# Kernel optimization log

Measured on AMD Instinct MI355X. Metric: run time of the kernel, lower is better.

The kernel has to match this reference:

```python
import jax, jax.numpy as jnp
import numpy as np

D_MODEL = 1024
N_HEADS = 16
HEAD_DIM = D_MODEL // N_HEADS


def setup_inputs() -> dict:
    key = jax.random.key(0)
    k_x, k_qkv, k_out = jax.random.split(key, 3)
    B, T = 4, 2048
    x = jax.random.normal(k_x, (B, T, D_MODEL), dtype=jnp.float32)
    # Linear(bias=False): y = x @ W, with W stored as [in, out]
    W_qkv = jax.random.normal(k_qkv, (D_MODEL, 3 * D_MODEL), dtype=jnp.float32) * (D_MODEL ** -0.5)
    W_out = jax.random.normal(k_out, (D_MODEL, D_MODEL), dtype=jnp.float32) * (D_MODEL ** -0.5)
    return {"x": x, "W_qkv": W_qkv, "W_out": W_out}


def reference(x, W_qkv, W_out):
    B, T, C = x.shape
    H, Dh = N_HEADS, HEAD_DIM
    scale = 1.0 / jnp.sqrt(jnp.asarray(Dh, dtype=x.dtype))

    qkv = x @ W_qkv  # [B,T,3C]
    q, k, v = jnp.split(qkv, 3, axis=-1)

    def split_heads(t):
        return t.reshape(B, T, H, Dh).transpose(0, 2, 1, 3)  # [B,H,T,Dh]

    q, k, v = split_heads(q), split_heads(k), split_heads(v)

    scores = jnp.einsum('bhqd,bhkd->bhqk', q, k) * scale  # [B,H,T,T]
    causal = jnp.tril(jnp.ones((T, T), dtype=bool))
    scores = jnp.where(causal, scores, jnp.asarray(-jnp.inf, dtype=scores.dtype))
    attn = jax.nn.softmax(scores, axis=-1)
    # dropout p=0.0 -> identity
    out = jnp.einsum('bhqk,bhkd->bhqd', attn, v)  # [B,H,T,Dh]
    out = out.transpose(0, 2, 1, 3).reshape(B, T, C)
    return out @ W_out
```

## Files before the change

### kernel.cpp

```cpp
#include <hip/hip_runtime.h>
#include <stdint.h>

typedef unsigned short u16;
typedef float f32x4 __attribute__((ext_vector_type(4)));
typedef short s16x8 __attribute__((ext_vector_type(8)));

#define SEQ 2048
#define DM 1024
#define NH 16
#define HD 64
#define BATCH 4
#define ROWS (BATCH*SEQ)
#define QTILES (SEQ/64)

__device__ __forceinline__ u16 f32_bf16(float f) {
  union { float f; uint32_t u; } c; c.f = f;
  uint32_t u = c.u;
  return (u16)((u + 0x7fffu + ((u >> 16) & 1u)) >> 16);
}
__device__ __forceinline__ u16 f32_bf16_trunc(float f) {
  union { float f; uint32_t u; } c; c.f = f;
  return (u16)(c.u >> 16);
}

#define GLOAD_LDS16(g, l) __builtin_amdgcn_global_load_lds( \
    (__attribute__((address_space(1))) void*)(g),           \
    (__attribute__((address_space(3))) void*)(l), 16, 0, 0)

__global__ __launch_bounds__(256) void cast_bf16_k(const float* __restrict__ in,
                                                   u16* __restrict__ out, int n4) {
  int i = blockIdx.x * 256 + threadIdx.x;
  if (i >= n4) return;
  float4 v = ((const float4*)in)[i];
  ushort4 o;
  o.x = f32_bf16(v.x); o.y = f32_bf16(v.y); o.z = f32_bf16(v.z); o.w = f32_bf16(v.w);
  ((ushort4*)out)[i] = o;
}

__global__ __launch_bounds__(256) void cast_transpose_k(const float* __restrict__ in,
                                                        u16* __restrict__ out, int R, int C) {
  __shared__ float tile[32][33];
  int c0 = blockIdx.x * 32, r0 = blockIdx.y * 32;
  int t = threadIdx.x;
  int lr = t >> 3, lc = (t & 7) * 4;
  float4 v = *(const float4*)(in + (size_t)(r0 + lr) * C + c0 + lc);
  tile[lr][lc] = v.x; tile[lr][lc + 1] = v.y; tile[lr][lc + 2] = v.z; tile[lr][lc + 3] = v.w;
  __syncthreads();
  ushort4 o;
  o.x = f32_bf16(tile[lc + 0][lr]);
  o.y = f32_bf16(tile[lc + 1][lr]);
  o.z = f32_bf16(tile[lc + 2][lr]);
  o.w = f32_bf16(tile[lc + 3][lr]);
  *(ushort4*)(out + (size_t)(c0 + lr) * R + r0 + lc) = o;
}

#define QSCALE 0.18033688011112042f


__device__ __forceinline__ f32x4 mfma16(s16x8 a, s16x8 b, f32x4 c) {
  return __builtin_amdgcn_mfma_f32_16x16x32_bf16(a, b, c, 0, 0, 0);
}

template<int STG, int ENDVM>
__device__ __forceinline__ void tile_body(
    const u16* lAc, const u16* lBc, u16* lAs, u16* lBs,
    const u16* gA0, const u16* gA1, const u16* gB0, const u16* gB1,
    int d0, int d1, int aoff, int boff, f32x4 (&acc)[8][4])
{
  s16x8 af[4], bfr[4];
#pragma unroll
  for (int ni = 0; ni < 4; ++ni) bfr[ni] = *(const s16x8*)&lBc[boff + ni * 512];
#pragma unroll
  for (int mi = 0; mi < 4; ++mi) af[mi] = *(const s16x8*)&lAc[aoff + mi * 512];
  if (STG) { GLOAD_LDS16(gA0, lAs + d0); GLOAD_LDS16(gA1, lAs + d1); }
  __builtin_amdgcn_s_barrier();
  asm volatile("s_waitcnt lgkmcnt(0)" ::: "memory");
  __builtin_amdgcn_sched_barrier(0);
  __builtin_amdgcn_s_setprio(1);
#pragma unroll
  for (int mi = 0; mi < 4; ++mi)
#pragma unroll
    for (int ni = 0; ni < 4; ++ni)
      acc[mi][ni] = mfma16(af[mi], bfr[ni], acc[mi][ni]);
  __builtin_amdgcn_s_setprio(0);
  __builtin_amdgcn_sched_barrier(0);
  __builtin_amdgcn_s_barrier();
#pragma unroll
  for (int mi = 0; mi < 4; ++mi) af[mi] = *(const s16x8*)&lAc[aoff + 2048 + mi * 512];
  if (STG) { GLOAD_LDS16(gB0, lBs + d0); GLOAD_LDS16(gB1, lBs + d1); }
  __builtin_amdgcn_s_barrier();
  asm volatile("s_waitcnt lgkmcnt(0)" ::: "memory");
  __builtin_amdgcn_sched_barrier(0);
  __builtin_amdgcn_s_setprio(1);
#pragma unroll
  for (int mi = 0; mi < 4; ++mi)
#pragma unroll
    for (int ni = 0; ni < 4; ++ni)
      acc[4 + mi][ni] = mfma16(af[mi], bfr[ni], acc[4 + mi][ni]);
  __builtin_amdgcn_s_setprio(0);
  __builtin_amdgcn_sched_barrier(0);
  if (ENDVM == 8)      asm volatile("s_waitcnt vmcnt(8)" ::: "memory");
  else if (ENDVM == 4) asm volatile("s_waitcnt vmcnt(4)" ::: "memory");
  else if (ENDVM == 0) asm volatile("s_waitcnt vmcnt(0)" ::: "memory");
  __builtin_amdgcn_s_barrier();
  __builtin_amdgcn_sched_barrier(0);
}

__global__ __launch_bounds__(512, 2) void qkv_gemm(
    const u16* __restrict__ A, const u16* __restrict__ Bt,
    u16* __restrict__ Qo, u16* __restrict__ Ko, u16* __restrict__ Vo)
{
  __shared__ u16 lA[4][8192];
  __shared__ u16 lB[4][8192];
  int t = threadIdx.x;

  int flat = blockIdx.y * 12 + blockIdx.x;
  int swz = (flat & 7) * 48 + (flat >> 3);
  int by = swz / 12, bx = swz - by * 12;
  int m0 = by * 256, n0 = bx * 256;

  int lane = t & 63, w = t >> 6;
  int m16 = lane & 15, quad = lane >> 4;
  int wm = w >> 2, wn = w & 3;

  int r0 = t >> 2;
  int scol = ((t & 3) ^ ((t >> 3) & 3)) * 8;
  const u16* Ag0 = A  + (size_t)(m0 + r0) * DM + scol;
  const u16* Ag1 = A  + (size_t)(m0 + 128 + r0) * DM + scol;
  const u16* Bg0 = Bt + (size_t)(n0 + r0) * DM + scol;
  const u16* Bg1 = Bt + (size_t)(n0 + 128 + r0) * DM + scol;
  int d0 = t * 8, d1 = 4096 + t * 8;

  int ka = (quad ^ ((m16 >> 1) & 3)) * 8;
  int aoff = (wm * 128 + m16) * 32 + ka;
  int boff = (wn * 64 + m16) * 32 + ka;

  f32x4 acc[8][4];
#pragma unroll
  for (int mi = 0; mi < 8; ++mi)
#pragma unroll
    for (int ni = 0; ni < 4; ++ni)
#pragma unroll
      for (int r = 0; r < 4; ++r) acc[mi][ni][r] = 0.f;

#pragma unroll
  for (int kt = 0; kt < 3; ++kt) {
    GLOAD_LDS16(Ag0 + kt * 32, lA[kt] + d0);
    GLOAD_LDS16(Ag1 + kt * 32, lA[kt] + d1);
    GLOAD_LDS16(Bg0 + kt * 32, lB[kt] + d0);
    GLOAD_LDS16(Bg1 + kt * 32, lB[kt] + d1);
  }
  asm volatile("s_waitcnt vmcnt(8)" ::: "memory");
  __builtin_amdgcn_s_barrier();
  __builtin_amdgcn_sched_barrier(0);

  for (int T = 0; T <= 28; ++T) {
    int cur = T & 3, stg = (T + 3) & 3;
    tile_body<1, 8>(lA[cur], lB[cur], lA[stg], lB[stg],
                    Ag0 + (T + 3) * 32, Ag1 + (T + 3) * 32,
                    Bg0 + (T + 3) * 32, Bg1 + (T + 3) * 32,
                    d0, d1, aoff, boff, acc);
  }
  tile_body<0, 4>(lA[1], lB[1], lA[0], lB[0], Ag0, Ag1, Bg0, Bg1, d0, d1, aoff, boff, acc);
  tile_body<0, 0>(lA[2], lB[2], lA[0], lB[0], Ag0, Ag1, Bg0, Bg1, d0, d1, aoff, boff, acc);
  tile_body<0, -1>(lA[3], lB[3], lA[0], lB[0], Ag0, Ag1, Bg0, Bg1, d0, d1, aoff, boff, acc);

#pragma unroll
  for (int mi = 0; mi < 8; ++mi) {
    int gr = m0 + wm * 128 + mi * 16 + quad * 4;
    int b = gr >> 11, tt = gr & 2047;
#pragma unroll
    for (int ni = 0; ni < 4; ++ni) {
      int gc = n0 + wn * 64 + ni * 16 + m16;
      int sec = gc >> 10, rem = gc & 1023, h = rem >> 6, d = rem & 63;
      if (sec == 0) {
#pragma unroll
        for (int r = 0; r < 4; ++r)
          Qo[(((size_t)b * NH + h) * SEQ + tt + r) * HD + d] = f32_bf16(acc[mi][ni][r] * QSCALE);
      } else if (sec == 1) {
#pragma unroll
        for (int r = 0; r < 4; ++r)
          Ko[(((size_t)b * NH + h) * SEQ + tt + r) * HD + d] = f32_bf16(acc[mi][ni][r]);
      } else {
        ushort4 o;
        o.x = f32_bf16(acc[mi][ni][0]); o.y = f32_bf16(acc[mi][ni][1]);
        o.z = f32_bf16(acc[mi][ni][2]); o.w = f32_bf16(acc[mi][ni][3]);
        *(ushort4*)&Vo[(((size_t)b * NH + h) * HD + d) * SEQ + tt] = o;
      }
    }
  }
}

template<int EPI>
__global__ __launch_bounds__(256) void gemm_bt(
    const u16* __restrict__ A, const u16* __restrict__ Bt,
    float* __restrict__ Cf, u16* __restrict__ Qo, u16* __restrict__ Ko, u16* __restrict__ Vo,
    int M, int N, int K)
{
  __shared__ u16 As[128 * 32];
  __shared__ u16 Bs[128 * 32];
  int t = threadIdx.x;
  int m0 = blockIdx.y * 128, n0 = blockIdx.x * 128;

  int srow = t >> 2, scol8 = (t & 3) * 8;
  const u16* Ag0 = A  + (size_t)(m0 + srow) * K + scol8;
  const u16* Ag1 = A  + (size_t)(m0 + 64 + srow) * K + scol8;
  const u16* Bg0 = Bt + (size_t)(n0 + srow) * K + scol8;
  const u16* Bg1 = Bt + (size_t)(n0 + 64 + srow) * K + scol8;
  u16* Al0 = As + t * 8;  u16* Al1 = As + 2048 + t * 8;
  u16* Bl0 = Bs + t * 8;  u16* Bl1 = Bs + 2048 + t * 8;

  int lane = t & 63, w = t >> 6;
  int m16 = lane & 15, quad = lane >> 4;
  int wr = (w >> 1) * 64, wc = (w & 1) * 64;

  f32x4 acc[4][4];
#pragma unroll
  for (int mi = 0; mi < 4; ++mi)
#pragma unroll
    for (int ni = 0; ni < 4; ++ni)
#pragma unroll
      for (int r = 0; r < 4; ++r) acc[mi][ni][r] = 0.f;

  for (int k0 = 0; k0 < K; k0 += 32) {
    __syncthreads();
    GLOAD_LDS16(Ag0 + k0, Al0);
    GLOAD_LDS16(Ag1 + k0, Al1);
    GLOAD_LDS16(Bg0 + k0, Bl0);
    GLOAD_LDS16(Bg1 + k0, Bl1);
    __syncthreads();
    s16x8 af[4], bf[4];
#pragma unroll
    for (int mi = 0; mi < 4; ++mi)
      af[mi] = *(const s16x8*)(As + (wr + mi * 16 + m16) * 32 + quad * 8);
#pragma unroll
    for (int ni = 0; ni < 4; ++ni)
      bf[ni] = *(const s16x8*)(Bs + (wc + ni * 16 + m16) * 32 + quad * 8);
#pragma unroll
    for (int mi = 0; mi < 4; ++mi)
#pragma unroll
      for (int ni = 0; ni < 4; ++ni)
        acc[mi][ni] = __builtin_amdgcn_mfma_f32_16x16x32_bf16(af[mi], bf[ni], acc[mi][ni], 0, 0, 0);
  }

  if (EPI == 0) {
#pragma unroll
    for (int mi = 0; mi < 4; ++mi) {
      int gr = m0 + wr + mi * 16 + quad * 4;
#pragma unroll
      for (int ni = 0; ni < 4; ++ni) {
        int gc = n0 + wc + ni * 16 + m16;
#pragma unroll
        for (int r = 0; r < 4; ++r)
          Cf[(size_t)(gr + r) * N + gc] = acc[mi][ni][r];
      }
    }
  } else {
#pragma unroll
    for (int mi = 0; mi < 4; ++mi) {
      int gr = m0 + wr + mi * 16 + quad * 4;
      int b = gr >> 11, tt = gr & 2047;
#pragma unroll
      for (int ni = 0; ni < 4; ++ni) {
        int gc = n0 + wc + ni * 16 + m16;
        int sec = gc >> 10, rem = gc & 1023, h = rem >> 6, d = rem & 63;
        if (sec == 0) {
#pragma unroll
          for (int r = 0; r < 4; ++r)
            Qo[(((size_t)b * NH + h) * SEQ + tt + r) * HD + d] = f32_bf16(acc[mi][ni][r] * QSCALE);
        } else if (sec == 1) {
#pragma unroll
          for (int r = 0; r < 4; ++r)
            Ko[(((size_t)b * NH + h) * SEQ + tt + r) * HD + d] = f32_bf16(acc[mi][ni][r]);
        } else {
          ushort4 o;
          o.x = f32_bf16(acc[mi][ni][0]); o.y = f32_bf16(acc[mi][ni][1]);
          o.z = f32_bf16(acc[mi][ni][2]); o.w = f32_bf16(acc[mi][ni][3]);
          *(ushort4*)&Vo[(((size_t)b * NH + h) * HD + d) * SEQ + tt] = o;
        }
      }
    }
  }
}

__global__ __launch_bounds__(256) void attn_k(
    const u16* __restrict__ Q, const u16* __restrict__ K,
    const u16* __restrict__ Vt_g,
    u16* __restrict__ O)
{
  __shared__ u16 Ks[64][72];
  __shared__ u16 Vt[64][72];
  __shared__ u16 Ps[4][16][72];
  int bh = blockIdx.y;
  int t = threadIdx.x, w = t >> 6, lane = t & 63;
  int m16 = lane & 15, quad = lane >> 4;
  int b = bh >> 4, h = bh & 15;

  int srow = t >> 2, sc = (t & 3) * 16;
  const u16* Kg0 = K    + ((size_t)bh * SEQ + srow) * HD  + sc;
  const u16* Vg0 = Vt_g + ((size_t)bh * HD  + srow) * SEQ + sc;

  for (int half = 0; half < 2; ++half) {
    int qt = half ? (QTILES - 1 - (int)blockIdx.x) : (int)blockIdx.x;
    int q0 = qt * 64;

    const u16* Qb = Q + ((size_t)bh * SEQ + q0 + w * 16 + m16) * HD + quad * 8;
    s16x8 qf0 = *(const s16x8*)Qb;
    s16x8 qf1 = *(const s16x8*)(Qb + 32);

    f32x4 acco[4];
    float l_part[4];
#pragma unroll
    for (int r = 0; r < 4; ++r) l_part[r] = 0.f;
#pragma unroll
    for (int ni = 0; ni < 4; ++ni)
#pragma unroll
      for (int r = 0; r < 4; ++r) acco[ni][r] = 0.f;

    for (int kt = 0; kt <= qt; ++kt) {
      uint4 kv0 = *(const uint4*)(Kg0 + (size_t)kt * 64 * HD);
      uint4 kv1 = *(const uint4*)(Kg0 + (size_t)kt * 64 * HD + 8);
      uint4 vv0 = *(const uint4*)(Vg0 + kt * 64);
      uint4 vv1 = *(const uint4*)(Vg0 + kt * 64 + 8);
      __syncthreads();
      *(uint4*)&Ks[srow][sc]     = kv0;
      *(uint4*)&Ks[srow][sc + 8] = kv1;
      *(uint4*)&Vt[srow][sc]     = vv0;
      *(uint4*)&Vt[srow][sc + 8] = vv1;
      __syncthreads();

      f32x4 sacc[4];
#pragma unroll
      for (int ni = 0; ni < 4; ++ni)
#pragma unroll
        for (int r = 0; r < 4; ++r) sacc[ni][r] = 0.f;
#pragma unroll
      for (int ni = 0; ni < 4; ++ni) {
        s16x8 kf0 = *(const s16x8*)&Ks[ni * 16 + m16][quad * 8];
        s16x8 kf1 = *(const s16x8*)&Ks[ni * 16 + m16][32 + quad * 8];
        sacc[ni] = __builtin_amdgcn_mfma_f32_16x16x32_bf16(qf0, kf0, sacc[ni], 0, 0, 0);
        sacc[ni] = __builtin_amdgcn_mfma_f32_16x16x32_bf16(qf1, kf1, sacc[ni], 0, 0, 0);
      }
      if (kt == qt) {
#pragma unroll
        for (int ni = 0; ni < 4; ++ni)
#pragma unroll
          for (int r = 0; r < 4; ++r)
            if (ni * 16 + m16 > w * 16 + quad * 4 + r) sacc[ni][r] = -1e30f;
      }

#pragma unroll
      for (int ni = 0; ni < 4; ++ni)
#pragma unroll
        for (int r = 0; r < 4; ++r) {
          float p = __builtin_amdgcn_exp2f(sacc[ni][r]);
          l_part[r] += p;
          Ps[w][quad * 4 + r][ni * 16 + m16] = f32_bf16_trunc(p);
        }

#pragma unroll
      for (int ks = 0; ks < 2; ++ks) {
        s16x8 pf = *(const s16x8*)&Ps[w][m16][ks * 32 + quad * 8];
#pragma unroll
        for (int ni = 0; ni < 4; ++ni) {
          s16x8 vf = *(const s16x8*)&Vt[ni * 16 + m16][ks * 32 + quad * 8];
          acco[ni] = __builtin_amdgcn_mfma_f32_16x16x32_bf16(pf, vf, acco[ni], 0, 0, 0);
        }
      }
    }

    float l[4];
#pragma unroll
    for (int r = 0; r < 4; ++r) l[r] = l_part[r];
#pragma unroll
    for (int off = 1; off < 16; off <<= 1)
#pragma unroll
      for (int r = 0; r < 4; ++r) l[r] += __shfl_xor(l[r], off, 64);

#pragma unroll
    for (int r = 0; r < 4; ++r) {
      float inv = 1.f / l[r];
      int trow = q0 + w * 16 + quad * 4 + r;
      size_t base = ((size_t)(b * SEQ + trow)) * DM + h * HD;
#pragma unroll
      for (int ni = 0; ni < 4; ++ni)
        O[base + ni * 16 + m16] = f32_bf16(acco[ni][r] * inv);
    }
  }
}

extern "C" void kernel_launch(void* const* d_in, const int* in_sizes, int n_in,
                              void* d_out, int out_size, void* d_ws, size_t ws_size,
                              hipStream_t stream) {
  const float* x    = (const float*)d_in[0];
  const float* Wqkv = (const float*)d_in[1];
  const float* Wout = (const float*)d_in[2];
  float* out = (float*)d_out;

  u16* ws = (u16*)d_ws;
  size_t off = 0;
  u16* x_bf   = ws + off; off += (size_t)ROWS * DM;
  u16* wqkv_t = ws + off; off += (size_t)(3 * DM) * DM;
  u16* wout_t = ws + off; off += (size_t)DM * DM;
  u16* Qb     = ws + off; off += (size_t)BATCH * NH * SEQ * HD;
  u16* Kb     = ws + off; off += (size_t)BATCH * NH * SEQ * HD;
  u16* Vb     = ws + off; off += (size_t)BATCH * NH * SEQ * HD;
  u16* AO     = ws + off; off += (size_t)ROWS * DM;

  cast_bf16_k<<<(ROWS * DM / 4 + 255) / 256, 256, 0, stream>>>(x, x_bf, ROWS * DM / 4);
  cast_transpose_k<<<dim3(3 * DM / 32, DM / 32), 256, 0, stream>>>(Wqkv, wqkv_t, DM, 3 * DM);
  cast_transpose_k<<<dim3(DM / 32, DM / 32), 256, 0, stream>>>(Wout, wout_t, DM, DM);
  qkv_gemm<<<dim3(12, 32), 512, 0, stream>>>(x_bf, wqkv_t, Qb, Kb, Vb);
  attn_k<<<dim3(QTILES / 2, BATCH * NH), 256, 0, stream>>>(Qb, Kb, Vb, AO);
  gemm_bt<0><<<dim3(DM / 128, ROWS / 128), 256, 0, stream>>>(
      AO, wout_t, out, nullptr, nullptr, nullptr, ROWS, DM, DM);
}
```

Before: 288.4 us.

## Prefetch next tile's LDS fragments across K-steps in QKV GEMM

```diff
diff --git a/kernel.cpp b/kernel.cpp
--- a/kernel.cpp
+++ b/kernel.cpp
@@ -61,48 +61,56 @@
   return __builtin_amdgcn_mfma_f32_16x16x32_bf16(a, b, c, 0, 0, 0);
 }
 
-template<int STG, int ENDVM>
-__device__ __forceinline__ void tile_body(
-    const u16* lAc, const u16* lBc, u16* lAs, u16* lBs,
+template<int STG, int ENDVM, int LAST>
+__device__ __forceinline__ void tile_step(
+    const u16* lAc, const u16* lBc,
+    const u16* lAn, const u16* lBn,
+    u16* lAs, u16* lBs,
     const u16* gA0, const u16* gA1, const u16* gB0, const u16* gB1,
-    int d0, int d1, int aoff, int boff, f32x4 (&acc)[8][4])
+    int d0, int d1, int aoff, int boff,
+    s16x8 (&fa)[4], s16x8 (&fb)[4],
+    s16x8 (&na)[4], s16x8 (&nb)[4],
+    f32x4 (&acc)[8][4])
 {
-  s16x8 af[4], bfr[4];
-#pragma unroll
-  for (int ni = 0; ni < 4; ++ni) bfr[ni] = *(const s16x8*)&lBc[boff + ni * 512];
-#pragma unroll
-  for (int mi = 0; mi < 4; ++mi) af[mi] = *(const s16x8*)&lAc[aoff + mi * 512];
+  __builtin_amdgcn_s_barrier();
+  __builtin_amdgcn_sched_barrier(0);
+  s16x8 f1[4];
+#pragma unroll
+  for (int mi = 0; mi < 4; ++mi) f1[mi] = *(const s16x8*)&lAc[aoff + 2048 + mi * 512];
   if (STG) { GLOAD_LDS16(gA0, lAs + d0); GLOAD_LDS16(gA1, lAs + d1); }
-  __builtin_amdgcn_s_barrier();
-  asm volatile("s_waitcnt lgkmcnt(0)" ::: "memory");
+  asm volatile("s_waitcnt lgkmcnt(4)" ::: "memory");
   __builtin_amdgcn_sched_barrier(0);
   __builtin_amdgcn_s_setprio(1);
 #pragma unroll
   for (int mi = 0; mi < 4; ++mi)
 #pragma unroll
     for (int ni = 0; ni < 4; ++ni)
-      acc[mi][ni] = mfma16(af[mi], bfr[ni], acc[mi][ni]);
+      acc[mi][ni] = mfma16(fa[mi], fb[ni], acc[mi][ni]);
   __builtin_amdgcn_s_setprio(0);
   __builtin_amdgcn_sched_barrier(0);
-  __builtin_amdgcn_s_barrier();
-#pragma unroll
-  for (int mi = 0; mi < 4; ++mi) af[mi] = *(const s16x8*)&lAc[aoff + 2048 + mi * 512];
   if (STG) { GLOAD_LDS16(gB0, lBs + d0); GLOAD_LDS16(gB1, lBs + d1); }
-  __builtin_amdgcn_s_barrier();
-  asm volatile("s_waitcnt lgkmcnt(0)" ::: "memory");
-  __builtin_amdgcn_sched_barrier(0);
-  __builtin_amdgcn_s_setprio(1);
-#pragma unroll
-  for (int mi = 0; mi < 4; ++mi)
-#pragma unroll
-    for (int ni = 0; ni < 4; ++ni)
-      acc[4 + mi][ni] = mfma16(af[mi], bfr[ni], acc[4 + mi][ni]);
-  __builtin_amdgcn_s_setprio(0);
-  __builtin_amdgcn_sched_barrier(0);
   if (ENDVM == 8)      asm volatile("s_waitcnt vmcnt(8)" ::: "memory");
   else if (ENDVM == 4) asm volatile("s_waitcnt vmcnt(4)" ::: "memory");
   else if (ENDVM == 0) asm volatile("s_waitcnt vmcnt(0)" ::: "memory");
   __builtin_amdgcn_s_barrier();
+  __builtin_amdgcn_sched_barrier(0);
+  if (!LAST) {
+#pragma unroll
+    for (int ni = 0; ni < 4; ++ni) nb[ni] = *(const s16x8*)&lBn[boff + ni * 512];
+#pragma unroll
+    for (int mi = 0; mi < 4; ++mi) na[mi] = *(const s16x8*)&lAn[aoff + mi * 512];
+    asm volatile("s_waitcnt lgkmcnt(8)" ::: "memory");
+  } else {
+    asm volatile("s_waitcnt lgkmcnt(0)" ::: "memory");
+  }
+  __builtin_amdgcn_sched_barrier(0);
+  __builtin_amdgcn_s_setprio(1);
+#pragma unroll
+  for (int mi = 0; mi < 4; ++mi)
+#pragma unroll
+    for (int ni = 0; ni < 4; ++ni)
+      acc[4 + mi][ni] = mfma16(f1[mi], fb[ni], acc[4 + mi][ni]);
+  __builtin_amdgcn_s_setprio(0);
   __builtin_amdgcn_sched_barrier(0);
 }
 
@@ -154,16 +162,34 @@
   __builtin_amdgcn_s_barrier();
   __builtin_amdgcn_sched_barrier(0);
 
-  for (int T = 0; T <= 28; ++T) {
-    int cur = T & 3, stg = (T + 3) & 3;
-    tile_body<1, 8>(lA[cur], lB[cur], lA[stg], lB[stg],
-                    Ag0 + (T + 3) * 32, Ag1 + (T + 3) * 32,
-                    Bg0 + (T + 3) * 32, Bg1 + (T + 3) * 32,
-                    d0, d1, aoff, boff, acc);
-  }
-  tile_body<0, 4>(lA[1], lB[1], lA[0], lB[0], Ag0, Ag1, Bg0, Bg1, d0, d1, aoff, boff, acc);
-  tile_body<0, 0>(lA[2], lB[2], lA[0], lB[0], Ag0, Ag1, Bg0, Bg1, d0, d1, aoff, boff, acc);
-  tile_body<0, -1>(lA[3], lB[3], lA[0], lB[0], Ag0, Ag1, Bg0, Bg1, d0, d1, aoff, boff, acc);
+  s16x8 fa0[4], fb0[4], fa1[4], fb1[4];
+#pragma unroll
+  for (int ni = 0; ni < 4; ++ni) fb0[ni] = *(const s16x8*)&lB[0][boff + ni * 512];
+#pragma unroll
+  for (int mi = 0; mi < 4; ++mi) fa0[mi] = *(const s16x8*)&lA[0][aoff + mi * 512];
+
+  for (int it = 0; it < 14; ++it) {
+    int T = 2 * it;
+    tile_step<1, 8, 0>(lA[T & 3], lB[T & 3], lA[(T + 1) & 3], lB[(T + 1) & 3],
+                       lA[(T + 3) & 3], lB[(T + 3) & 3],
+                       Ag0 + (T + 3) * 32, Ag1 + (T + 3) * 32,
+                       Bg0 + (T + 3) * 32, Bg1 + (T + 3) * 32,
+                       d0, d1, aoff, boff, fa0, fb0, fa1, fb1, acc);
+    tile_step<1, 8, 0>(lA[(T + 1) & 3], lB[(T + 1) & 3], lA[(T + 2) & 3], lB[(T + 2) & 3],
+                       lA[(T + 4) & 3], lB[(T + 4) & 3],
+                       Ag0 + (T + 4) * 32, Ag1 + (T + 4) * 32,
+                       Bg0 + (T + 4) * 32, Bg1 + (T + 4) * 32,
+                       d0, d1, aoff, boff, fa1, fb1, fa0, fb0, acc);
+  }
+  tile_step<1, 8, 0>(lA[0], lB[0], lA[1], lB[1], lA[3], lB[3],
+                     Ag0 + 31 * 32, Ag1 + 31 * 32, Bg0 + 31 * 32, Bg1 + 31 * 32,
+                     d0, d1, aoff, boff, fa0, fb0, fa1, fb1, acc);
+  tile_step<0, 4, 0>(lA[1], lB[1], lA[2], lB[2], lA[0], lB[0],
+                     Ag0, Ag1, Bg0, Bg1, d0, d1, aoff, boff, fa1, fb1, fa0, fb0, acc);
+  tile_step<0, 0, 0>(lA[2], lB[2], lA[3], lB[3], lA[0], lB[0],
+                     Ag0, Ag1, Bg0, Bg1, d0, d1, aoff, boff, fa0, fb0, fa1, fb1, acc);
+  tile_step<0, -1, 1>(lA[3], lB[3], lA[0], lB[0], lA[0], lB[0],
+                      Ag0, Ag1, Bg0, Bg1, d0, d1, aoff, boff, fa1, fb1, fa0, fb0, acc);
 
 #pragma unroll
   for (int mi = 0; mi < 8; ++mi) {
```

Result: faster. 281.0 us (-2.5%).
